# Performance work log

Measured on AMD Instinct MI355X. Metric: run time of the kernel, lower is better.

Reference implementation:

```python
import jax, jax.numpy as jnp
import numpy as np

NUM_MODULES = 4
EXPERTS_PER_MODULE = 4
TOTAL_EXPERTS = NUM_MODULES * EXPERTS_PER_MODULE
TOP_K = 4
NORM_TOPK_PROB = True
T = 32768
D = 1536


def setup_inputs() -> dict:
    key = jax.random.key(0)
    k1, k2, k3 = jax.random.split(key, 3)
    hidden_states = jax.random.normal(k1, (T, D), dtype=jnp.float32)
    # nn.Linear weights: (out_features, in_features)
    Wm = jax.random.normal(k2, (NUM_MODULES, D), dtype=jnp.float32) * 0.02
    We = jax.random.normal(k3, (TOTAL_EXPERTS, D), dtype=jnp.float32) * 0.02
    return {"hidden_states": hidden_states, "Wm": Wm, "We": We}


def reference(hidden_states, Wm, We):
    Tn = hidden_states.shape[0]
    # Stage 1: module routing
    module_logits = jnp.einsum('td,md->tm', hidden_states, Wm)  # (T, num_modules)
    module_probs = jax.nn.softmax(module_logits.astype(jnp.float32), axis=-1)
    # Stage 2: expert routing, grouped per module (intra-module softmax)
    expert_logits = jnp.einsum('td,ed->te', hidden_states, We)  # (T, total_experts)
    expert_logits = expert_logits.reshape(Tn, NUM_MODULES, EXPERTS_PER_MODULE)
    expert_probs = jax.nn.softmax(expert_logits.astype(jnp.float32), axis=-1)
    # Combined hierarchical distribution
    combined_probs = (module_probs[:, :, None] * expert_probs).reshape(Tn, TOTAL_EXPERTS)
    # Top-k over flat combined distribution
    top_k_weights, top_k_indices = jax.lax.top_k(combined_probs, TOP_K)
    if NORM_TOPK_PROB:
        top_k_weights = top_k_weights / (jnp.sum(top_k_weights, axis=-1, keepdims=True) + 1e-8)
    top_k_weights = top_k_weights.astype(hidden_states.dtype)
    return combined_probs, top_k_weights, top_k_indices
```

## Files before the change

kernel.cpp:

```cpp
#include <hip/hip_runtime.h>
#include <math.h>


#define DD 1536
#define NM 4
#define NE 16
#define NW 20
#define RPB 64
#define NWAVE 8
#define NTHR (NWAVE * 64)
#define CPW 192
#define CHUNK 16
#define NCHUNK (CPW / CHUNK)
#define LSTRIDE 20
#define HS_FLOATS (RPB * LSTRIDE)
#define W_FLOATS  (NW * LSTRIDE)
#define WAVE_REG  (HS_FLOATS + W_FLOATS)

typedef float v4f __attribute__((ext_vector_type(4)));

union SharedMem {
    float stage[NWAVE * WAVE_REG];
    float xch[NW * NTHR];
};

__global__ __launch_bounds__(NTHR)
void router_kernel(const float* __restrict__ hs,
                   const float* __restrict__ Wm,
                   const float* __restrict__ We,
                   float* __restrict__ out,
                   int T)
{
    __shared__ SharedMem sm;
    const int tid  = threadIdx.x;
    const int wv   = tid >> 6;
    const int lane = tid & 63;
    const int rowBlock = blockIdx.x * RPB;
    const int colStart = wv * CPW;

    float acc[NW];
#pragma unroll
    for (int e = 0; e < NW; e++) acc[e] = 0.f;

    const int srow = lane >> 2;
    const int scol = (lane & 3) << 2;
    const float* hsBase = hs + (size_t)(rowBlock + srow) * DD + colStart + scol;
    float* myHs = &sm.stage[wv * WAVE_REG];
    float* myW  = myHs + HS_FLOATS;

    const int wrow0 = lane >> 2;
    const int wgrp0 = (lane & 3) << 2;
    const float* weBase = We + (size_t)wrow0 * DD + colStart + wgrp0;
    const float* wmBase = Wm + (size_t)(lane >> 2) * DD + colStart + wgrp0;

    v4f hbuf[4], wbuf0, wbuf1;
#pragma unroll
    for (int i = 0; i < 4; i++)
        hbuf[i] = *(const v4f*)(hsBase + (size_t)(i * 16) * DD);
    wbuf0 = *(const v4f*)(weBase);
    if (lane < 16) wbuf1 = *(const v4f*)(wmBase);

    for (int c = 0; c < CPW; c += CHUNK) {
#pragma unroll
        for (int i = 0; i < 4; i++)
            *(v4f*)&myHs[(srow + i * 16) * LSTRIDE + scol] = hbuf[i];
        *(v4f*)&myW[wrow0 * LSTRIDE + wgrp0] = wbuf0;
        if (lane < 16)
            *(v4f*)&myW[(16 + (lane >> 2)) * LSTRIDE + wgrp0] = wbuf1;

        if (c + CHUNK < CPW) {
            const int cn = c + CHUNK;
#pragma unroll
            for (int i = 0; i < 4; i++)
                hbuf[i] = *(const v4f*)(hsBase + (size_t)(i * 16) * DD + cn);
            wbuf0 = *(const v4f*)(weBase + cn);
            if (lane < 16) wbuf1 = *(const v4f*)(wmBase + cn);
        }

#pragma unroll
        for (int g = 0; g < 4; g++) {
            v4f h = *(const v4f*)&myHs[lane * LSTRIDE + (g << 2)];
#pragma unroll
            for (int e = 0; e < NW; e++) {
                v4f w = *(const v4f*)&myW[e * LSTRIDE + (g << 2)];
                acc[e] += h.x * w.x + h.y * w.y + h.z * w.z + h.w * w.w;
            }
        }
    }

    __syncthreads();
#pragma unroll
    for (int e = 0; e < NW; e++) sm.xch[e * NTHR + tid] = acc[e];
    __syncthreads();

    if (wv == 0) {
        float logit[NW];
#pragma unroll
        for (int e = 0; e < NW; e++) {
            float s = 0.f;
#pragma unroll
            for (int w = 0; w < NWAVE; w++)
                s += sm.xch[e * NTHR + w * 64 + lane];
            logit[e] = s;
        }

        float mmax = logit[16];
#pragma unroll
        for (int m = 1; m < NM; m++) mmax = fmaxf(mmax, logit[16 + m]);
        float mexp[NM], msum = 0.f;
#pragma unroll
        for (int m = 0; m < NM; m++) { mexp[m] = expf(logit[16 + m] - mmax); msum += mexp[m]; }

        float comb[NE];
#pragma unroll
        for (int m = 0; m < NM; m++) {
            float mprob = mexp[m] / msum;
            float emax = logit[m * 4];
#pragma unroll
            for (int j = 1; j < 4; j++) emax = fmaxf(emax, logit[m * 4 + j]);
            float ee[4], esum = 0.f;
#pragma unroll
            for (int j = 0; j < 4; j++) { ee[j] = expf(logit[m * 4 + j] - emax); esum += ee[j]; }
            float scale = mprob / esum;
#pragma unroll
            for (int j = 0; j < 4; j++) comb[m * 4 + j] = ee[j] * scale;
        }

        const int row = rowBlock + lane;
        float4* cw = (float4*)(out + (size_t)row * 16);
        cw[0] = make_float4(comb[0],  comb[1],  comb[2],  comb[3]);
        cw[1] = make_float4(comb[4],  comb[5],  comb[6],  comb[7]);
        cw[2] = make_float4(comb[8],  comb[9],  comb[10], comb[11]);
        cw[3] = make_float4(comb[12], comb[13], comb[14], comb[15]);

        float tv[4]; int ti[4];
        unsigned mask = 0;
#pragma unroll
        for (int k = 0; k < 4; k++) {
            float best = -1.f; int bi = 0;
#pragma unroll
            for (int i = 0; i < NE; i++) {
                bool avail = !((mask >> i) & 1u);
                if (avail && comb[i] > best) { best = comb[i]; bi = i; }
            }
            tv[k] = best; ti[k] = bi; mask |= 1u << bi;
        }
        float s = tv[0] + tv[1] + tv[2] + tv[3] + 1e-8f;

        const size_t wOff = (size_t)T * 16;
        const size_t iOff = (size_t)T * 20;
        float4* ww = (float4*)(out + wOff + (size_t)row * 4);
        *ww = make_float4(tv[0] / s, tv[1] / s, tv[2] / s, tv[3] / s);
        float4* iw = (float4*)(out + iOff + (size_t)row * 4);
        *iw = make_float4((float)ti[0], (float)ti[1], (float)ti[2], (float)ti[3]);
    }
}

extern "C" void kernel_launch(void* const* d_in, const int* in_sizes, int n_in,
                              void* d_out, int out_size, void* d_ws, size_t ws_size,
                              hipStream_t stream)
{
    const float* hs = (const float*)d_in[0];
    const float* Wm = (const float*)d_in[1];
    const float* We = (const float*)d_in[2];
    float* out = (float*)d_out;
    const int T = in_sizes[0] / DD;
    router_kernel<<<T / RPB, NTHR, 0, stream>>>(hs, Wm, We, out, T);
}
```

Before: 296.2 us.

## Process two rows per lane with 128-row blocks and narrower staging chunks

Each block now covers 128 rows and each lane accumulates two rows, so every weight vector read from LDS is reused for two dot products. This is meant to cut LDS weight traffic per FMA and halve the number of blocks that reload the weights. The staging chunk is narrowed to 8 columns with a 12-float stride, We and Wm loads are merged into one 40-lane load, and the reduction and epilogue run twice. The cost is doubled accumulator registers, which may lower occupancy, plus an extra reduction round with its barriers.

```diff
diff --git a/kernel.cpp b/kernel.cpp
--- a/kernel.cpp
+++ b/kernel.cpp
@@ -6,15 +6,14 @@
 #define NM 4
 #define NE 16
 #define NW 20
-#define RPB 64
+#define RPB 128
 #define NWAVE 8
 #define NTHR (NWAVE * 64)
 #define CPW 192
-#define CHUNK 16
-#define NCHUNK (CPW / CHUNK)
-#define LSTRIDE 20
-#define HS_FLOATS (RPB * LSTRIDE)
-#define W_FLOATS  (NW * LSTRIDE)
+#define CHUNK 8
+#define STRIDE 12
+#define HS_FLOATS (RPB * STRIDE)
+#define W_FLOATS  (NW * STRIDE)
 #define WAVE_REG  (HS_FLOATS + W_FLOATS)
 
 typedef float v4f __attribute__((ext_vector_type(4)));
@@ -23,6 +22,70 @@
     float stage[NWAVE * WAVE_REG];
     float xch[NW * NTHR];
 };
+
+__device__ __forceinline__ void epilogue(const float* __restrict__ xch,
+                                         int lane, int row,
+                                         float* __restrict__ out, int T)
+{
+    float logit[NW];
+#pragma unroll
+    for (int e = 0; e < NW; e++) {
+        float s = 0.f;
+#pragma unroll
+        for (int w = 0; w < NWAVE; w++)
+            s += xch[e * NTHR + w * 64 + lane];
+        logit[e] = s;
+    }
+
+    float mmax = logit[16];
+#pragma unroll
+    for (int m = 1; m < NM; m++) mmax = fmaxf(mmax, logit[16 + m]);
+    float mexp[NM], msum = 0.f;
+#pragma unroll
+    for (int m = 0; m < NM; m++) { mexp[m] = expf(logit[16 + m] - mmax); msum += mexp[m]; }
+
+    float comb[NE];
+#pragma unroll
+    for (int m = 0; m < NM; m++) {
+        float mprob = mexp[m] / msum;
+        float emax = logit[m * 4];
+#pragma unroll
+        for (int j = 1; j < 4; j++) emax = fmaxf(emax, logit[m * 4 + j]);
+        float ee[4], esum = 0.f;
+#pragma unroll
+        for (int j = 0; j < 4; j++) { ee[j] = expf(logit[m * 4 + j] - emax); esum += ee[j]; }
+        float scale = mprob / esum;
+#pragma unroll
+        for (int j = 0; j < 4; j++) comb[m * 4 + j] = ee[j] * scale;
+    }
+
+    float4* cw = (float4*)(out + (size_t)row * 16);
+    cw[0] = make_float4(comb[0],  comb[1],  comb[2],  comb[3]);
+    cw[1] = make_float4(comb[4],  comb[5],  comb[6],  comb[7]);
+    cw[2] = make_float4(comb[8],  comb[9],  comb[10], comb[11]);
+    cw[3] = make_float4(comb[12], comb[13], comb[14], comb[15]);
+
+    float tv[4]; int ti[4];
+    unsigned mask = 0;
+#pragma unroll
+    for (int k = 0; k < 4; k++) {
+        float best = -1.f; int bi = 0;
+#pragma unroll
+        for (int i = 0; i < NE; i++) {
+            bool avail = !((mask >> i) & 1u);
+            if (avail && comb[i] > best) { best = comb[i]; bi = i; }
+        }
+        tv[k] = best; ti[k] = bi; mask |= 1u << bi;
+    }
+    float s = tv[0] + tv[1] + tv[2] + tv[3] + 1e-8f;
+
+    const size_t wOff = (size_t)T * 16;
+    const size_t iOff = (size_t)T * 20;
+    float4* ww = (float4*)(out + wOff + (size_t)row * 4);
+    *ww = make_float4(tv[0] / s, tv[1] / s, tv[2] / s, tv[3] / s);
+    float4* iw = (float4*)(out + iOff + (size_t)row * 4);
+    *iw = make_float4((float)ti[0], (float)ti[1], (float)ti[2], (float)ti[3]);
+}
 
 __global__ __launch_bounds__(NTHR)
 void router_kernel(const float* __restrict__ hs,
@@ -38,122 +101,67 @@
     const int rowBlock = blockIdx.x * RPB;
     const int colStart = wv * CPW;
 
-    float acc[NW];
+    float acc0[NW], acc1[NW];
 #pragma unroll
-    for (int e = 0; e < NW; e++) acc[e] = 0.f;
+    for (int e = 0; e < NW; e++) { acc0[e] = 0.f; acc1[e] = 0.f; }
 
-    const int srow = lane >> 2;
-    const int scol = (lane & 3) << 2;
+    const int srow = lane >> 1;
+    const int scol = (lane & 1) << 2;
     const float* hsBase = hs + (size_t)(rowBlock + srow) * DD + colStart + scol;
     float* myHs = &sm.stage[wv * WAVE_REG];
     float* myW  = myHs + HS_FLOATS;
 
-    const int wrow0 = lane >> 2;
-    const int wgrp0 = (lane & 3) << 2;
-    const float* weBase = We + (size_t)wrow0 * DD + colStart + wgrp0;
-    const float* wmBase = Wm + (size_t)(lane >> 2) * DD + colStart + wgrp0;
+    const int wrow = (lane >> 1) < 20 ? (lane >> 1) : 19;
+    const int wgrp = (lane & 1) << 2;
+    const float* wPtr = ((wrow < 16) ? (We + (size_t)wrow * DD)
+                                     : (Wm + (size_t)(wrow - 16) * DD))
+                        + colStart + wgrp;
+    const bool wLane = (lane < 40);
 
-    v4f hbuf[4], wbuf0, wbuf1;
+    v4f hbuf[4], wbuf;
 #pragma unroll
     for (int i = 0; i < 4; i++)
-        hbuf[i] = *(const v4f*)(hsBase + (size_t)(i * 16) * DD);
-    wbuf0 = *(const v4f*)(weBase);
-    if (lane < 16) wbuf1 = *(const v4f*)(wmBase);
+        hbuf[i] = *(const v4f*)(hsBase + (size_t)(i * 32) * DD);
+    if (wLane) wbuf = *(const v4f*)(wPtr);
 
+#pragma unroll 1
     for (int c = 0; c < CPW; c += CHUNK) {
 #pragma unroll
         for (int i = 0; i < 4; i++)
-            *(v4f*)&myHs[(srow + i * 16) * LSTRIDE + scol] = hbuf[i];
-        *(v4f*)&myW[wrow0 * LSTRIDE + wgrp0] = wbuf0;
-        if (lane < 16)
-            *(v4f*)&myW[(16 + (lane >> 2)) * LSTRIDE + wgrp0] = wbuf1;
+            *(v4f*)&myHs[(srow + i * 32) * STRIDE + scol] = hbuf[i];
+        if (wLane) *(v4f*)&myW[wrow * STRIDE + wgrp] = wbuf;
 
         if (c + CHUNK < CPW) {
             const int cn = c + CHUNK;
 #pragma unroll
             for (int i = 0; i < 4; i++)
-                hbuf[i] = *(const v4f*)(hsBase + (size_t)(i * 16) * DD + cn);
-            wbuf0 = *(const v4f*)(weBase + cn);
-            if (lane < 16) wbuf1 = *(const v4f*)(wmBase + cn);
+                hbuf[i] = *(const v4f*)(hsBase + (size_t)(i * 32) * DD + cn);
+            if (wLane) wbuf = *(const v4f*)(wPtr + cn);
         }
 
 #pragma unroll
-        for (int g = 0; g < 4; g++) {
-            v4f h = *(const v4f*)&myHs[lane * LSTRIDE + (g << 2)];
+        for (int g = 0; g < 2; g++) {
+            v4f h0 = *(const v4f*)&myHs[lane * STRIDE + (g << 2)];
+            v4f h1 = *(const v4f*)&myHs[(lane + 64) * STRIDE + (g << 2)];
 #pragma unroll
             for (int e = 0; e < NW; e++) {
-                v4f w = *(const v4f*)&myW[e * LSTRIDE + (g << 2)];
-                acc[e] += h.x * w.x + h.y * w.y + h.z * w.z + h.w * w.w;
+                v4f w = *(const v4f*)&myW[e * STRIDE + (g << 2)];
+                acc0[e] += h0.x * w.x + h0.y * w.y + h0.z * w.z + h0.w * w.w;
+                acc1[e] += h1.x * w.x + h1.y * w.y + h1.z * w.z + h1.w * w.w;
             }
         }
     }
 
     __syncthreads();
 #pragma unroll
-    for (int e = 0; e < NW; e++) sm.xch[e * NTHR + tid] = acc[e];
+    for (int e = 0; e < NW; e++) sm.xch[e * NTHR + tid] = acc0[e];
     __syncthreads();
-
-    if (wv == 0) {
-        float logit[NW];
+    if (wv == 0) epilogue(sm.xch, lane, rowBlock + lane, out, T);
+    __syncthreads();
 #pragma unroll
-        for (int e = 0; e < NW; e++) {
-            float s = 0.f;
-#pragma unroll
-            for (int w = 0; w < NWAVE; w++)
-                s += sm.xch[e * NTHR + w * 64 + lane];
-            logit[e] = s;
-        }
-
-        float mmax = logit[16];
-#pragma unroll
-        for (int m = 1; m < NM; m++) mmax = fmaxf(mmax, logit[16 + m]);
-        float mexp[NM], msum = 0.f;
-#pragma unroll
-        for (int m = 0; m < NM; m++) { mexp[m] = expf(logit[16 + m] - mmax); msum += mexp[m]; }
-
-        float comb[NE];
-#pragma unroll
-        for (int m = 0; m < NM; m++) {
-            float mprob = mexp[m] / msum;
-            float emax = logit[m * 4];
-#pragma unroll
-            for (int j = 1; j < 4; j++) emax = fmaxf(emax, logit[m * 4 + j]);
-            float ee[4], esum = 0.f;
-#pragma unroll
-            for (int j = 0; j < 4; j++) { ee[j] = expf(logit[m * 4 + j] - emax); esum += ee[j]; }
-            float scale = mprob / esum;
-#pragma unroll
-            for (int j = 0; j < 4; j++) comb[m * 4 + j] = ee[j] * scale;
-        }
-
-        const int row = rowBlock + lane;
-        float4* cw = (float4*)(out + (size_t)row * 16);
-        cw[0] = make_float4(comb[0],  comb[1],  comb[2],  comb[3]);
-        cw[1] = make_float4(comb[4],  comb[5],  comb[6],  comb[7]);
-        cw[2] = make_float4(comb[8],  comb[9],  comb[10], comb[11]);
-        cw[3] = make_float4(comb[12], comb[13], comb[14], comb[15]);
-
-        float tv[4]; int ti[4];
-        unsigned mask = 0;
-#pragma unroll
-        for (int k = 0; k < 4; k++) {
-            float best = -1.f; int bi = 0;
-#pragma unroll
-            for (int i = 0; i < NE; i++) {
-                bool avail = !((mask >> i) & 1u);
-                if (avail && comb[i] > best) { best = comb[i]; bi = i; }
-            }
-            tv[k] = best; ti[k] = bi; mask |= 1u << bi;
-        }
-        float s = tv[0] + tv[1] + tv[2] + tv[3] + 1e-8f;
-
-        const size_t wOff = (size_t)T * 16;
-        const size_t iOff = (size_t)T * 20;
-        float4* ww = (float4*)(out + wOff + (size_t)row * 4);
-        *ww = make_float4(tv[0] / s, tv[1] / s, tv[2] / s, tv[3] / s);
-        float4* iw = (float4*)(out + iOff + (size_t)row * 4);
-        *iw = make_float4((float)ti[0], (float)ti[1], (float)ti[2], (float)ti[3]);
-    }
+    for (int e = 0; e < NW; e++) sm.xch[e * NTHR + tid] = acc1[e];
+    __syncthreads();
+    if (wv == 0) epilogue(sm.xch, lane, rowBlock + 64 + lane, out, T);
 }
 
 extern "C" void kernel_launch(void* const* d_in, const int* in_sizes, int n_in,
```

Result: slower. 303.6 us (+2.5%).
